# Kernel tuning notes

Measured on AMD Instinct MI355X. Metric: run time of the kernel, lower is better.

The kernel has to match this reference:

```python
import jax, jax.numpy as jnp
import numpy as np

T_STEPS, B, NMUL = 365, 20000, 4
NEARZERO = 1e-06

_BOUNDS = {
    'parBETA': (1.0, 6.0), 'parFC': (50.0, 1000.0), 'parK0': (0.05, 0.9),
    'parK1': (0.01, 0.5), 'parK2': (0.001, 0.2), 'parLP': (0.2, 1.0),
    'parPERC': (0.0, 10.0), 'parUZL': (0.0, 100.0), 'parTT': (-2.5, 2.5),
    'parCFMAX': (0.5, 10.0), 'parCFR': (0.0, 0.1), 'parCWH': (0.0, 0.2),
    'parBETAET': (0.3, 5.0), 'parC': (0.0, 1.0),
}


def setup_inputs() -> dict:
    key = jax.random.key(0)
    kf, kt, kp, *pkeys = jax.random.split(key, 3 + len(_BOUNDS))
    # forcing (T, B, 3): [prcp (mm/d), tmean (degC), pet (mm/d)]
    prcp = jax.random.uniform(kf, (T_STEPS, B), jnp.float32) * 10.0
    tmean = jax.random.normal(kt, (T_STEPS, B), jnp.float32) * 10.0
    pet = jax.random.uniform(kp, (T_STEPS, B), jnp.float32) * 5.0
    inp = {'forcing': jnp.stack([prcp, tmean, pet], axis=-1)}
    for k_rng, (name, (lo, hi)) in zip(pkeys, _BOUNDS.items()):
        inp[name] = jax.random.uniform(k_rng, (B, NMUL), jnp.float32, lo, hi)
    return inp


def _hbv_scan(forcing, parTT, parCFMAX, parCFR, parCWH, parFC, parBETA, parLP,
              parBETAET, parC, parPERC, parK0, parK1, parK2, parUZL):
    eps = NEARZERO
    nmul = parTT.shape[-1]
    n_grid = forcing.shape[1]
    # expand forcing to (T, B, nmul)
    Pm = jnp.broadcast_to(forcing[:, :, 0:1], forcing.shape[:2] + (nmul,))
    Tm = jnp.broadcast_to(forcing[:, :, 1:2], forcing.shape[:2] + (nmul,))
    PETm = jnp.broadcast_to(forcing[:, :, 2:3], forcing.shape[:2] + (nmul,))

    snow0 = jnp.full((n_grid, nmul), eps, forcing.dtype)
    zeros = jnp.zeros((n_grid, nmul), forcing.dtype)

    def step(carry, x):
        snow, melt, sm, suz, slz = carry
        p, t_val, pet = x
        temp_diff = t_val - parTT
        is_rain = temp_diff > 0.0
        rain = jnp.where(is_rain, p, 0.0)
        snow_input = jnp.where(is_rain, 0.0, p)
        snow1 = snow + snow_input
        pot_melt = parCFMAX * jnp.maximum(temp_diff, 0.0)
        melt_amount = jnp.minimum(pot_melt, snow1)
        snow2 = snow1 - melt_amount
        melt1 = melt + melt_amount
        pot_refreeze = parCFR * parCFMAX * jnp.maximum(-temp_diff, 0.0)
        refreeze = jnp.minimum(pot_refreeze, melt1)
        snow_out = snow2 + refreeze
        melt2 = melt1 - refreeze
        tosoil = jnp.maximum(melt2 - parCWH * snow_out, 0.0)
        melt_out = melt2 - tosoil
        soil_wet = jnp.clip(jnp.power(jnp.maximum(sm / parFC, eps), parBETA), 0.0, 1.0)
        recharge = (rain + tosoil) * soil_wet
        sm1 = sm + rain + tosoil - recharge
        excess = jnp.maximum(sm1 - parFC, 0.0)
        sm2 = sm1 - excess
        ef1 = jnp.clip(sm2 / (parLP * parFC), 0.0, 1.0)
        evapfactor = jnp.clip(jnp.power(jnp.maximum(ef1, eps), parBETAET), 0.0, 1.0)
        etact = jnp.minimum(pet * evapfactor, sm2)
        sm_ae = jnp.maximum(sm2 - etact, eps)
        sm_ratio = jnp.minimum(sm_ae / parFC, 1.0)
        capillary = jnp.minimum(slz, parC * slz * (1.0 - sm_ratio))
        sm_out = jnp.maximum(sm_ae + capillary, eps)
        slz_ac = jnp.maximum(slz - capillary, eps)
        suz1 = suz + recharge + excess
        perc_flux = jnp.minimum(suz1, parPERC)
        suz2 = suz1 - perc_flux
        slz1 = slz_ac + perc_flux
        q0 = parK0 * jnp.maximum(suz2 - parUZL, 0.0)
        suz3 = suz2 - q0
        q1 = parK1 * suz3
        suz_out = suz3 - q1
        q2 = parK2 * slz1
        slz_out = slz1 - q2
        q = q0 + q1 + q2
        return (snow_out, melt_out, sm_out, suz_out, slz_out), q

    _, Qsim = jax.lax.scan(step, (snow0, zeros, zeros, zeros, zeros), (Pm, Tm, PETm))
    return Qsim  # (T, B, nmul)


def reference(forcing, parTT, parCFMAX, parCFR, parCWH, parFC, parBETA, parLP,
              parBETAET, parC, parPERC, parK0, parK1, parK2, parUZL):
    Qsim = _hbv_scan(forcing, parTT, parCFMAX, parCFR, parCWH, parFC, parBETA,
                     parLP, parBETAET, parC, parPERC, parK0, parK1, parK2, parUZL)
    Qsim_avg = Qsim.mean(axis=-1)  # 'streamflow' (T, B)
    return (Qsim_avg, Qsim)
```

## Files before the change

kernel.cpp:

```cpp
#include <hip/hip_runtime.h>

#define TSTEPS 365
#define BGRID  20000
#define NMUL   4
#define NEARZERO 1e-6f
#define PF 8

struct F3 { float p, t, pet; };

__device__ __forceinline__ float quad_sum(float x) {
    int a = __builtin_amdgcn_update_dpp(0, __float_as_int(x),
                                        0xB1 , 0xF, 0xF, true);
    float s1 = x + __int_as_float(a);
    int b = __builtin_amdgcn_update_dpp(0, __float_as_int(s1),
                                        0x4E , 0xF, 0xF, true);
    return s1 + __int_as_float(b);
}

__device__ __forceinline__ float fast_log2(float x) { return __builtin_amdgcn_logf(x); }
__device__ __forceinline__ float fast_exp2(float x) { return __builtin_amdgcn_exp2f(x); }

__global__ __launch_bounds__(64) __attribute__((amdgpu_waves_per_eu(2, 2)))
void hbv_fwd(
    const float* __restrict__ forcing,
    const float* __restrict__ pBETA,  const float* __restrict__ pFC,
    const float* __restrict__ pK0,    const float* __restrict__ pK1,
    const float* __restrict__ pK2,    const float* __restrict__ pLP,
    const float* __restrict__ pPERC,  const float* __restrict__ pUZL,
    const float* __restrict__ pTT,    const float* __restrict__ pCFMAX,
    const float* __restrict__ pCFR,   const float* __restrict__ pCWH,
    const float* __restrict__ pBETAET,const float* __restrict__ pC,
    float* __restrict__ out_avg,
    float* __restrict__ out_q)
{
    const int tid = blockIdx.x * 64 + threadIdx.x;
    const int b = tid >> 2;

    const float parBETA   = pBETA[tid];
    const float parFC     = pFC[tid];
    const float parK0     = pK0[tid];
    const float parK1     = pK1[tid];
    const float parK2     = pK2[tid];
    const float parLP     = pLP[tid];
    const float parPERC   = pPERC[tid];
    const float parUZL    = pUZL[tid];
    const float parTT     = pTT[tid];
    const float parCFMAX  = pCFMAX[tid];
    const float parCFR    = pCFR[tid];
    const float parCWH    = pCWH[tid];
    const float parBETAET = pBETAET[tid];
    const float parC      = pC[tid];

    const float refreeze_coef = parCFR * parCFMAX;
    const float inv_FC   = 1.0f / parFC;
    const float inv_LPFC = 1.0f / (parLP * parFC);

    float snow = NEARZERO, melt = 0.0f, sm = 0.0f, suz = 0.0f, slz = 0.0f;

    const F3* __restrict__ fp = (const F3*)forcing + b;
    float* __restrict__ qq = out_q + tid;
    float* __restrict__ qa = out_avg + b;

    F3 buf[PF];
#pragma unroll
    for (int i = 0; i < PF; ++i) { buf[i] = *fp; fp += BGRID; }

    auto step = [&](const F3 fv) {
        const float p   = fv.p;
        const float tv  = fv.t;
        const float pet = fv.pet;

        const float temp_diff = tv - parTT;
        const bool  is_rain = temp_diff > 0.0f;
        const float rain       = is_rain ? p : 0.0f;
        const float snow_input = is_rain ? 0.0f : p;
        float snow1 = snow + snow_input;
        const float pot_melt = parCFMAX * fmaxf(temp_diff, 0.0f);
        const float melt_amount = fminf(pot_melt, snow1);
        snow1 -= melt_amount;
        float melt1 = melt + melt_amount;
        const float pot_refreeze = refreeze_coef * fmaxf(-temp_diff, 0.0f);
        const float refreeze = fminf(pot_refreeze, melt1);
        snow = snow1 + refreeze;
        melt1 -= refreeze;
        const float tosoil = fmaxf(melt1 - parCWH * snow, 0.0f);
        melt = melt1 - tosoil;

        const float x1 = fmaxf(sm * inv_FC, NEARZERO);
        const float soil_wet = fminf(fast_exp2(parBETA * fast_log2(x1)), 1.0f);
        const float rt = rain + tosoil;
        const float recharge = rt * soil_wet;
        float sm1 = sm + rt - recharge;
        const float excess = fmaxf(sm1 - parFC, 0.0f);
        sm1 -= excess;
        const float ef1 = fminf(sm1 * inv_LPFC, 1.0f);
        const float x2 = fmaxf(ef1, NEARZERO);
        const float evapfactor = fminf(fast_exp2(parBETAET * fast_log2(x2)), 1.0f);
        const float etact = fminf(pet * evapfactor, sm1);
        const float sm_ae = fmaxf(sm1 - etact, NEARZERO);
        const float sm_ratio = fminf(sm_ae * inv_FC, 1.0f);
        const float capillary = fminf(slz, parC * slz * (1.0f - sm_ratio));
        sm = fmaxf(sm_ae + capillary, NEARZERO);
        float slz1 = fmaxf(slz - capillary, NEARZERO);

        float suz1 = suz + recharge + excess;
        const float perc_flux = fminf(suz1, parPERC);
        suz1 -= perc_flux;
        slz1 += perc_flux;
        const float q0 = parK0 * fmaxf(suz1 - parUZL, 0.0f);
        suz1 -= q0;
        const float q1 = parK1 * suz1;
        suz = suz1 - q1;
        const float q2 = parK2 * slz1;
        slz = slz1 - q2;
        const float q = q0 + q1 + q2;

        *qq = q;
        qq += BGRID * NMUL;
        const float qs = quad_sum(q);
        *qa = qs * 0.25f;
        qa += BGRID;
    };

    constexpr int MAINC = ((TSTEPS - PF) / PF) * PF;
#pragma clang loop unroll(disable)
    for (int base = 0; base < MAINC; base += PF) {
#pragma unroll
        for (int j = 0; j < PF; ++j) {
            const F3 fv = buf[j];
            buf[j] = *fp; fp += BGRID;
            step(fv);
        }
    }
#pragma unroll
    for (int j = 0; j < PF; ++j) {
        const F3 fv = buf[j];
        if (j < TSTEPS - MAINC - PF) { buf[j] = *fp; fp += BGRID; }
        step(fv);
    }
#pragma unroll
    for (int j = 0; j < TSTEPS - MAINC - PF; ++j) {
        step(buf[j]);
    }
}

extern "C" void kernel_launch(void* const* d_in, const int* in_sizes, int n_in,
                              void* d_out, int out_size, void* d_ws, size_t ws_size,
                              hipStream_t stream) {
    const float* forcing = (const float*)d_in[0];

    float* out_avg = (float*)d_out;
    float* out_q   = out_avg + (size_t)TSTEPS * BGRID;

    const int total = BGRID * NMUL;
    const int block = 64;
    const int grid  = total / block;
    hbv_fwd<<<grid, block, 0, stream>>>(forcing,
        (const float*)d_in[1], (const float*)d_in[2], (const float*)d_in[3],
        (const float*)d_in[4], (const float*)d_in[5], (const float*)d_in[6],
        (const float*)d_in[7], (const float*)d_in[8], (const float*)d_in[9],
        (const float*)d_in[10], (const float*)d_in[11], (const float*)d_in[12],
        (const float*)d_in[13], (const float*)d_in[14],
        out_avg, out_q);
}
```

Measured before the change: 301.5 us.

## Process two nmul members per thread with pair-swap reduction

Each thread now handles two of the four nmul members of a grid cell, interleaved as c0 and c0+2, so the thread count is halved. Each thread gets two independent recurrence chains to overlap, and each forcing load is shared across two members. The quad reduction becomes an in-thread add followed by a single DPP pair swap. The prefetch depth drops from 8 to 4 and the waves-per-EU hint is relaxed. The trade-off is half as many wavefronts (625 blocks of 64), more registers per thread, and stride-2 output stores that are less coalesced.

```diff
diff --git a/kernel.cpp b/kernel.cpp
--- a/kernel.cpp
+++ b/kernel.cpp
@@ -4,23 +4,21 @@
 #define BGRID  20000
 #define NMUL   4
 #define NEARZERO 1e-6f
-#define PF 8
+#define PF 4
+#define V  2
 
 struct F3 { float p, t, pet; };
 
-__device__ __forceinline__ float quad_sum(float x) {
+__device__ __forceinline__ float pair_swap(float x) {
     int a = __builtin_amdgcn_update_dpp(0, __float_as_int(x),
                                         0xB1 , 0xF, 0xF, true);
-    float s1 = x + __int_as_float(a);
-    int b = __builtin_amdgcn_update_dpp(0, __float_as_int(s1),
-                                        0x4E , 0xF, 0xF, true);
-    return s1 + __int_as_float(b);
+    return __int_as_float(a);
 }
 
 __device__ __forceinline__ float fast_log2(float x) { return __builtin_amdgcn_logf(x); }
 __device__ __forceinline__ float fast_exp2(float x) { return __builtin_amdgcn_exp2f(x); }
 
-__global__ __launch_bounds__(64) __attribute__((amdgpu_waves_per_eu(2, 2)))
+__global__ __launch_bounds__(64) __attribute__((amdgpu_waves_per_eu(1, 2)))
 void hbv_fwd(
     const float* __restrict__ forcing,
     const float* __restrict__ pBETA,  const float* __restrict__ pFC,
@@ -34,31 +32,34 @@
     float* __restrict__ out_q)
 {
     const int tid = blockIdx.x * 64 + threadIdx.x;
-    const int b = tid >> 2;
+    const int b  = tid >> 1;
+    const int c0 = (b << 2) + (tid & 1);
 
-    const float parBETA   = pBETA[tid];
-    const float parFC     = pFC[tid];
-    const float parK0     = pK0[tid];
-    const float parK1     = pK1[tid];
-    const float parK2     = pK2[tid];
-    const float parLP     = pLP[tid];
-    const float parPERC   = pPERC[tid];
-    const float parUZL    = pUZL[tid];
-    const float parTT     = pTT[tid];
-    const float parCFMAX  = pCFMAX[tid];
-    const float parCFR    = pCFR[tid];
-    const float parCWH    = pCWH[tid];
-    const float parBETAET = pBETAET[tid];
-    const float parC      = pC[tid];
+    float parBETA[V], parFC[V], parK0[V], parK1[V], parK2[V], parPERC[V],
+          parUZL[V], parTT[V], parCFMAX[V], parCWH[V], parBETAET[V], parC[V],
+          refreeze_coef[V], inv_FC[V], inv_LPFC[V];
+#pragma unroll
+    for (int v = 0; v < V; ++v) {
+        const int c = c0 + 2 * v;
+        parBETA[v]   = pBETA[c];   parFC[v]   = pFC[c];
+        parK0[v]     = pK0[c];     parK1[v]   = pK1[c];
+        parK2[v]     = pK2[c];     parPERC[v] = pPERC[c];
+        parUZL[v]    = pUZL[c];    parTT[v]   = pTT[c];
+        parCFMAX[v]  = pCFMAX[c];  parCWH[v]  = pCWH[c];
+        parBETAET[v] = pBETAET[c]; parC[v]    = pC[c];
+        refreeze_coef[v] = pCFR[c] * parCFMAX[v];
+        inv_FC[v]   = 1.0f / parFC[v];
+        inv_LPFC[v] = 1.0f / (pLP[c] * parFC[v]);
+    }
 
-    const float refreeze_coef = parCFR * parCFMAX;
-    const float inv_FC   = 1.0f / parFC;
-    const float inv_LPFC = 1.0f / (parLP * parFC);
-
-    float snow = NEARZERO, melt = 0.0f, sm = 0.0f, suz = 0.0f, slz = 0.0f;
+    float snow[V], melt[V], sm[V], suz[V], slz[V];
+#pragma unroll
+    for (int v = 0; v < V; ++v) {
+        snow[v] = NEARZERO; melt[v] = 0.0f; sm[v] = 0.0f; suz[v] = 0.0f; slz[v] = 0.0f;
+    }
 
     const F3* __restrict__ fp = (const F3*)forcing + b;
-    float* __restrict__ qq = out_q + tid;
+    float* __restrict__ qq = out_q + c0;
     float* __restrict__ qa = out_avg + b;
 
     F3 buf[PF];
@@ -66,58 +67,60 @@
     for (int i = 0; i < PF; ++i) { buf[i] = *fp; fp += BGRID; }
 
     auto step = [&](const F3 fv) {
-        const float p   = fv.p;
-        const float tv  = fv.t;
-        const float pet = fv.pet;
+        float q[V];
+#pragma unroll
+        for (int v = 0; v < V; ++v) {
+            const float temp_diff = fv.t - parTT[v];
+            const bool  is_rain = temp_diff > 0.0f;
+            const float rain       = is_rain ? fv.p : 0.0f;
+            const float snow_input = is_rain ? 0.0f : fv.p;
+            float snow1 = snow[v] + snow_input;
+            const float pot_melt = parCFMAX[v] * fmaxf(temp_diff, 0.0f);
+            const float melt_amount = fminf(pot_melt, snow1);
+            snow1 -= melt_amount;
+            float melt1 = melt[v] + melt_amount;
+            const float pot_refreeze = refreeze_coef[v] * fmaxf(-temp_diff, 0.0f);
+            const float refreeze = fminf(pot_refreeze, melt1);
+            snow[v] = snow1 + refreeze;
+            melt1 -= refreeze;
+            const float tosoil = fmaxf(melt1 - parCWH[v] * snow[v], 0.0f);
+            melt[v] = melt1 - tosoil;
 
-        const float temp_diff = tv - parTT;
-        const bool  is_rain = temp_diff > 0.0f;
-        const float rain       = is_rain ? p : 0.0f;
-        const float snow_input = is_rain ? 0.0f : p;
-        float snow1 = snow + snow_input;
-        const float pot_melt = parCFMAX * fmaxf(temp_diff, 0.0f);
-        const float melt_amount = fminf(pot_melt, snow1);
-        snow1 -= melt_amount;
-        float melt1 = melt + melt_amount;
-        const float pot_refreeze = refreeze_coef * fmaxf(-temp_diff, 0.0f);
-        const float refreeze = fminf(pot_refreeze, melt1);
-        snow = snow1 + refreeze;
-        melt1 -= refreeze;
-        const float tosoil = fmaxf(melt1 - parCWH * snow, 0.0f);
-        melt = melt1 - tosoil;
+            const float x1 = fmaxf(sm[v] * inv_FC[v], NEARZERO);
+            const float soil_wet = fminf(fast_exp2(parBETA[v] * fast_log2(x1)), 1.0f);
+            const float rt = rain + tosoil;
+            const float recharge = rt * soil_wet;
+            float sm1 = sm[v] + rt - recharge;
+            const float excess = fmaxf(sm1 - parFC[v], 0.0f);
+            sm1 -= excess;
+            const float ef1 = fminf(sm1 * inv_LPFC[v], 1.0f);
+            const float x2 = fmaxf(ef1, NEARZERO);
+            const float evapfactor = fminf(fast_exp2(parBETAET[v] * fast_log2(x2)), 1.0f);
+            const float etact = fminf(fv.pet * evapfactor, sm1);
+            const float sm_ae = fmaxf(sm1 - etact, NEARZERO);
+            const float sm_ratio = fminf(sm_ae * inv_FC[v], 1.0f);
+            const float capillary = fminf(slz[v], parC[v] * slz[v] * (1.0f - sm_ratio));
+            sm[v] = fmaxf(sm_ae + capillary, NEARZERO);
+            float slz1 = fmaxf(slz[v] - capillary, NEARZERO);
 
-        const float x1 = fmaxf(sm * inv_FC, NEARZERO);
-        const float soil_wet = fminf(fast_exp2(parBETA * fast_log2(x1)), 1.0f);
-        const float rt = rain + tosoil;
-        const float recharge = rt * soil_wet;
-        float sm1 = sm + rt - recharge;
-        const float excess = fmaxf(sm1 - parFC, 0.0f);
-        sm1 -= excess;
-        const float ef1 = fminf(sm1 * inv_LPFC, 1.0f);
-        const float x2 = fmaxf(ef1, NEARZERO);
-        const float evapfactor = fminf(fast_exp2(parBETAET * fast_log2(x2)), 1.0f);
-        const float etact = fminf(pet * evapfactor, sm1);
-        const float sm_ae = fmaxf(sm1 - etact, NEARZERO);
-        const float sm_ratio = fminf(sm_ae * inv_FC, 1.0f);
-        const float capillary = fminf(slz, parC * slz * (1.0f - sm_ratio));
-        sm = fmaxf(sm_ae + capillary, NEARZERO);
-        float slz1 = fmaxf(slz - capillary, NEARZERO);
+            float suz1 = suz[v] + recharge + excess;
+            const float perc_flux = fminf(suz1, parPERC[v]);
+            suz1 -= perc_flux;
+            slz1 += perc_flux;
+            const float q0 = parK0[v] * fmaxf(suz1 - parUZL[v], 0.0f);
+            suz1 -= q0;
+            const float q1 = parK1[v] * suz1;
+            suz[v] = suz1 - q1;
+            const float q2 = parK2[v] * slz1;
+            slz[v] = slz1 - q2;
+            q[v] = q0 + q1 + q2;
+        }
 
-        float suz1 = suz + recharge + excess;
-        const float perc_flux = fminf(suz1, parPERC);
-        suz1 -= perc_flux;
-        slz1 += perc_flux;
-        const float q0 = parK0 * fmaxf(suz1 - parUZL, 0.0f);
-        suz1 -= q0;
-        const float q1 = parK1 * suz1;
-        suz = suz1 - q1;
-        const float q2 = parK2 * slz1;
-        slz = slz1 - q2;
-        const float q = q0 + q1 + q2;
-
-        *qq = q;
+        qq[0] = q[0];
+        qq[2] = q[1];
         qq += BGRID * NMUL;
-        const float qs = quad_sum(q);
+        const float h  = q[0] + q[1];
+        const float qs = h + pair_swap(h);
         *qa = qs * 0.25f;
         qa += BGRID;
     };
@@ -152,7 +155,7 @@
     float* out_avg = (float*)d_out;
     float* out_q   = out_avg + (size_t)TSTEPS * BGRID;
 
-    const int total = BGRID * NMUL;
+    const int total = BGRID * NMUL / V;
     const int block = 64;
     const int grid  = total / block;
     hbv_fwd<<<grid, block, 0, stream>>>(forcing,
```

Measured after the change: 295.2 us. -2.1%, faster.
